# Optimization experiments

Hardware: AMD Instinct MI355X
Metric: run time of the kernel (lower is better)

## Reference

```python
import jax, jax.numpy as jnp
import numpy as np

PAD = float(-2**32 + 1)


def setup_inputs() -> dict:
    key = jax.random.key(0)
    ks = jax.random.split(key, 10)
    B, S, D = 8, 1024, 1024
    s = 0.02  # keep projections in sane range
    return {
        "Q": jax.random.normal(ks[0], (B, S, D), jnp.float32),
        "K": jax.random.normal(ks[1], (B, S, D), jnp.float32),
        "V": jax.random.normal(ks[2], (B, S, D), jnp.float32),
        "WQ": jax.random.normal(ks[3], (D, D), jnp.float32) * s,
        "bQ": jnp.zeros((D,), jnp.float32),
        "WK": jax.random.normal(ks[4], (D, D), jnp.float32) * s,
        "bK": jnp.zeros((D,), jnp.float32),
        "WV": jax.random.normal(ks[5], (D, D), jnp.float32) * s,
        "bV": jnp.zeros((D,), jnp.float32),
        "WO": jax.random.normal(ks[6], (D, D), jnp.float32) * s,
        "bO": jnp.zeros((D,), jnp.float32),
        "h": 16,
    }


def reference(Q, K, V, WQ, bQ, WK, bK, WV, bV, WO, bO, h):
    B, S, D = Q.shape
    dk = D // h
    # Dense projections with relu activation (as in the Keras layer)
    Qp = jax.nn.relu(Q @ WQ + bQ)
    Kp = jax.nn.relu(K @ WK + bK)
    Vp = jax.nn.relu(V @ WV + bV)
    # tf.concat(tf.split(x, h, axis=2), axis=0): head-major stacking -> (h, B, S, dk)
    qh = Qp.reshape(B, S, h, dk).transpose(2, 0, 1, 3)
    kh = Kp.reshape(B, S, h, dk).transpose(2, 0, 1, 3)
    vh = Vp.reshape(B, S, h, dk).transpose(2, 0, 1, 3)
    # scaled dot product; NOTE: source scales by 1/sqrt(d_model), not 1/sqrt(d_k)
    scores = jnp.einsum('hbqd,hbkd->hbqk', qh, kh) / jnp.sqrt(jnp.float32(D))
    # key padding mask: zero key rows -> large negative
    kmask = jnp.sum(jnp.abs(kh), axis=-1) != 0  # (h,B,Tk)
    scores = jnp.where(kmask[:, :, None, :], scores, PAD)
    w = jax.nn.softmax(scores, axis=-1)
    # query padding mask: zero query rows -> zero weights
    qmask = jnp.sign(jnp.sum(jnp.abs(qh), axis=-1))  # (h,B,Tq), 0/1
    w = w * qmask[:, :, :, None]
    # dropout_prob = 0.0 -> identity
    out = jnp.einsum('hbqk,hbkd->hbqd', w, vh)
    # tf.concat(tf.split(dot_product, h, axis=0), axis=2) -> (B,S,h*dk)
    out = out.transpose(1, 2, 0, 3).reshape(B, S, D)
    return jax.nn.relu(out @ WO + bO)
```

## Files before the change

kernel.cpp:

```cpp
#include <hip/hip_runtime.h>
#include <hip/hip_bf16.h>
#include <cstdint>

#define DEV __device__ __forceinline__

typedef __attribute__((ext_vector_type(4))) float f32x4;
typedef __attribute__((ext_vector_type(8))) short b16x8;
typedef __attribute__((ext_vector_type(4))) unsigned short u16x4;
typedef __attribute__((ext_vector_type(8))) unsigned short u16x8;
typedef __attribute__((ext_vector_type(2))) unsigned int u32x2;
typedef __attribute__((ext_vector_type(4))) unsigned int u32x4;

typedef __attribute__((address_space(1))) void gvoid_t;
typedef __attribute__((address_space(3))) void lvoid_t;

static constexpr int Bsz = 8, Ssz = 1024, Dsz = 1024;
static constexpr int Mrows = Bsz * Ssz;

DEV void gld16(const void* g, void* l) {
  __builtin_amdgcn_global_load_lds((gvoid_t*)(uintptr_t)g,
                                   (lvoid_t*)(unsigned)(uintptr_t)l, 16, 0, 0);
}

DEV unsigned short f2bf(float x) {
  unsigned int u = __float_as_uint(x);
  u += 0x7fffu + ((u >> 16) & 1u);
  return (unsigned short)(u >> 16);
}

DEV unsigned int cvt2(float lo, float hi) {
  __hip_bfloat162 h = __float22bfloat162_rn(make_float2(lo, hi));
  unsigned int u;
  __builtin_memcpy(&u, &h, 4);
  return u;
}

DEV float fexp2(float x) {
#if __has_builtin(__builtin_amdgcn_exp2f)
  return __builtin_amdgcn_exp2f(x);
#else
  return exp2f(x);
#endif
}

__global__ __launch_bounds__(256) void wconv_kernel(
    const float* __restrict__ WQ, const float* __restrict__ WK,
    const float* __restrict__ WV, const float* __restrict__ WO,
    unsigned short* __restrict__ Wt) {
  __shared__ float tile[64][65];
  const int w = blockIdx.z;
  const float* W = (w == 0) ? WQ : (w == 1) ? WK : (w == 2) ? WV : WO;
  const int k0 = blockIdx.x * 64, n0 = blockIdx.y * 64;
  const int t = threadIdx.x;
  {
    const int r = t >> 4;
    const int c = (t & 15) * 4;
#pragma unroll
    for (int i = 0; i < 4; ++i) {
      f32x4 v = *(const f32x4*)(W + (size_t)(k0 + i * 16 + r) * Dsz + n0 + c);
      tile[i * 16 + r][c + 0] = v[0];
      tile[i * 16 + r][c + 1] = v[1];
      tile[i * 16 + r][c + 2] = v[2];
      tile[i * 16 + r][c + 3] = v[3];
    }
  }
  __syncthreads();
  {
    const int n = t >> 2;
    const int ks = (t & 3) * 16;
    unsigned short* dst =
        Wt + (size_t)w * Dsz * Dsz + (size_t)(n0 + n) * Dsz + k0 + ks;
#pragma unroll
    for (int j = 0; j < 16; j += 4) {
      u16x4 p;
#pragma unroll
      for (int jj = 0; jj < 4; ++jj) p[jj] = f2bf(tile[ks + j + jj][n]);
      *(u16x4*)(dst + j) = p;
    }
  }
}

template <int OUT_MODE>
DEV void gemm_body_f32(unsigned short* __restrict__ Asl,
                       unsigned short* __restrict__ Bsl,
                       const float* __restrict__ A,
                       const unsigned short* __restrict__ Bt,
                       const float* __restrict__ bias, void* __restrict__ C_,
                       int m0, int n0, float outscale) {
  constexpr int Kd = 1024, Nd = 1024;
  const int t = threadIdx.x, lane = t & 63, wave = t >> 6;
  const int grp = lane >> 4, r16 = lane & 15;
  const int wm = wave >> 2, wn = wave & 3;
  const int swz = (r16 & 7) << 4;
  f32x4 acc[4][4] = {};
  f32x4 areg[2][2];

  auto loadA = [&](int kt) {
#pragma unroll
    for (int it = 0; it < 2; ++it) {
      int chunk = it * 512 + t;
      int row = chunk >> 3, c = chunk & 7;
      int csw = c ^ (row & 7);
      const float* src = A + (size_t)(m0 + row) * Kd + kt + csw * 8;
      areg[it][0] = *(const f32x4*)src;
      areg[it][1] = *(const f32x4*)(src + 4);
    }
  };
  auto writeA = [&]() {
#pragma unroll
    for (int it = 0; it < 2; ++it) {
      int chunk = it * 512 + t;
      u32x4 w;
      w[0] = cvt2(areg[it][0][0], areg[it][0][1]);
      w[1] = cvt2(areg[it][0][2], areg[it][0][3]);
      w[2] = cvt2(areg[it][1][0], areg[it][1][1]);
      w[3] = cvt2(areg[it][1][2], areg[it][1][3]);
      *(u32x4*)((char*)Asl + chunk * 16) = w;
    }
  };
  auto stageB = [&](int kt, int pb) {
#pragma unroll
    for (int j = 0; j < 4; ++j) {
      int chunk = (wave * 4 + j) * 64 + lane;
      int row = chunk >> 3, c = chunk & 7;
      int csw = c ^ (row & 7);
      gld16(Bt + (size_t)(n0 + row) * Kd + kt + csw * 8,
            (char*)Bsl + pb * 32768 + (wave * 4 + j) * 1024);
    }
  };

  loadA(0);
  stageB(0, 0);
  int cur = 0;
  for (int kt = 0; kt < Kd; kt += 64) {
    writeA();
    __syncthreads();
    if (kt < Kd - 64) {
      stageB(kt + 64, cur ^ 1);
      loadA(kt + 64);
    }
#pragma unroll
    for (int cs = 0; cs < 2; ++cs) {
      b16x8 af[4], bfr[4];
#pragma unroll
      for (int mi = 0; mi < 4; ++mi)
        af[mi] = *(const b16x8*)((char*)Asl + (wm * 64 + mi * 16 + r16) * 128 +
                                 ((cs * 64 + grp * 16) ^ swz));
#pragma unroll
      for (int ni = 0; ni < 4; ++ni)
        bfr[ni] = *(const b16x8*)((char*)Bsl + cur * 32768 +
                                  (wn * 64 + ni * 16 + r16) * 128 +
                                  ((cs * 64 + grp * 16) ^ swz));
#pragma unroll
      for (int mi = 0; mi < 4; ++mi)
#pragma unroll
        for (int ni = 0; ni < 4; ++ni)
          acc[mi][ni] = __builtin_amdgcn_mfma_f32_16x16x32_bf16(
              af[mi], bfr[ni], acc[mi][ni], 0, 0, 0);
    }
    __syncthreads();
    cur ^= 1;
  }
#pragma unroll
  for (int mi = 0; mi < 4; ++mi) {
#pragma unroll
    for (int ni = 0; ni < 4; ++ni) {
      int col = n0 + wn * 64 + ni * 16 + r16;
      float bv = bias[col];
      int row0 = m0 + wm * 64 + mi * 16 + grp * 4;
      if constexpr (OUT_MODE == 2) {
        int bb = row0 >> 10, s = row0 & 1023;
        u16x4 pk;
#pragma unroll
        for (int r = 0; r < 4; ++r)
          pk[r] = f2bf(fmaxf(acc[mi][ni][r] + bv, 0.0f) * outscale);
        *(u16x4*)((unsigned short*)C_ +
                  (((size_t)(bb * 1024 + col)) << 10) + s) = pk;
      } else {
#pragma unroll
        for (int r = 0; r < 4; ++r) {
          float v = fmaxf(acc[mi][ni][r] + bv, 0.0f) * outscale;
          ((unsigned short*)C_)[(size_t)(row0 + r) * Nd + col] = f2bf(v);
        }
      }
    }
  }
}

DEV void gemm_body_bf16(unsigned short* __restrict__ Asl,
                        unsigned short* __restrict__ Bsl,
                        const unsigned short* __restrict__ A,
                        const unsigned short* __restrict__ Bt,
                        const float* __restrict__ bias, float* __restrict__ C_,
                        int m0, int n0) {
  constexpr int Kd = 1024, Nd = 1024;
  const int t = threadIdx.x, lane = t & 63, wave = t >> 6;
  const int grp = lane >> 4, r16 = lane & 15;
  const int wm = wave >> 1, wn = wave & 1;
  const int swz = (r16 & 7) << 4;
  f32x4 acc[4][4] = {};
  for (int kt = 0; kt < Kd; kt += 64) {
#pragma unroll
    for (int j = 0; j < 4; ++j) {
      int chunk = (wave * 4 + j) * 64 + lane;
      int row = chunk >> 3, c = chunk & 7;
      int csw = c ^ (row & 7);
      gld16(Bt + (size_t)(n0 + row) * Kd + kt + csw * 8,
            (char*)Bsl + (wave * 4 + j) * 1024);
      gld16(A + (size_t)(m0 + row) * Kd + kt + csw * 8,
            (char*)Asl + (wave * 4 + j) * 1024);
    }
    __syncthreads();
#pragma unroll
    for (int cs = 0; cs < 2; ++cs) {
      b16x8 af[4], bfr[4];
#pragma unroll
      for (int mi = 0; mi < 4; ++mi)
        af[mi] = *(const b16x8*)((char*)Asl + (wm * 64 + mi * 16 + r16) * 128 +
                                 ((cs * 64 + grp * 16) ^ swz));
#pragma unroll
      for (int ni = 0; ni < 4; ++ni)
        bfr[ni] = *(const b16x8*)((char*)Bsl + (wn * 64 + ni * 16 + r16) * 128 +
                                  ((cs * 64 + grp * 16) ^ swz));
#pragma unroll
      for (int mi = 0; mi < 4; ++mi)
#pragma unroll
        for (int ni = 0; ni < 4; ++ni)
          acc[mi][ni] = __builtin_amdgcn_mfma_f32_16x16x32_bf16(
              af[mi], bfr[ni], acc[mi][ni], 0, 0, 0);
    }
    __syncthreads();
  }
#pragma unroll
  for (int mi = 0; mi < 4; ++mi) {
#pragma unroll
    for (int ni = 0; ni < 4; ++ni) {
      int col = n0 + wn * 64 + ni * 16 + r16;
      float bv = bias[col];
      int row0 = m0 + wm * 64 + mi * 16 + grp * 4;
#pragma unroll
      for (int r = 0; r < 4; ++r) {
        float v = fmaxf(acc[mi][ni][r] + bv, 0.0f);
        C_[(size_t)(row0 + r) * Nd + col] = v;
      }
    }
  }
}

static constexpr float QSCALE = 0.03125f * 1.4426950408889634f;

__global__ __launch_bounds__(512) void proj3_kernel(
    const float* __restrict__ Q, const float* __restrict__ K,
    const float* __restrict__ V, const unsigned short* __restrict__ Wt,
    const float* __restrict__ bQ, const float* __restrict__ bK,
    const float* __restrict__ bV, unsigned short* __restrict__ Qp,
    unsigned short* __restrict__ Kp, unsigned short* __restrict__ VpT) {
  __shared__ unsigned short Asl[128 * 64] __attribute__((aligned(16)));
  __shared__ unsigned short Bsl[2 * 256 * 64] __attribute__((aligned(16)));
  const size_t DD = (size_t)Dsz * Dsz;
  const int bid = blockIdx.x;
  const int id2 = (bid & 7) * 32 + (bid >> 3);
  const int n0 = (id2 & 3) * 256, m0 = (id2 >> 2) * 128;
  const int z = blockIdx.z;
  if (z == 0)
    gemm_body_f32<1>(Asl, Bsl, Q, Wt, bQ, Qp, m0, n0, QSCALE);
  else if (z == 1)
    gemm_body_f32<1>(Asl, Bsl, K, Wt + DD, bK, Kp, m0, n0, 1.0f);
  else
    gemm_body_f32<2>(Asl, Bsl, V, Wt + 2 * DD, bV, VpT, m0, n0, 1.0f);
}

__global__ __launch_bounds__(256) void out_gemm_kernel(
    const unsigned short* __restrict__ AO,
    const unsigned short* __restrict__ WOt, const float* __restrict__ bO,
    float* __restrict__ Out) {
  __shared__ unsigned short Asl[128 * 64] __attribute__((aligned(16)));
  __shared__ unsigned short Bsl[128 * 64] __attribute__((aligned(16)));
  const int bid = blockIdx.x;
  const int id2 = (bid & 7) * 64 + (bid >> 3);
  const int n0 = (id2 & 7) * 128, m0 = (id2 >> 3) * 128;
  gemm_body_bf16(Asl, Bsl, AO, WOt, bO, Out, m0, n0);
}

__global__ __launch_bounds__(512, 4) void attn_kernel(
    const unsigned short* __restrict__ Qp, const unsigned short* __restrict__ Kp,
    const unsigned short* __restrict__ VpT, unsigned short* __restrict__ AO) {
  __shared__ unsigned short Ks[2][64 * 64] __attribute__((aligned(16)));
  __shared__ unsigned short Vs[2][64 * 64] __attribute__((aligned(16)));
  __shared__ unsigned short Ps[16][16 * 64] __attribute__((aligned(16)));
  const int t = threadIdx.x, lane = t & 63, wave = t >> 6;
  const int grp = lane >> 4, r16 = lane & 15;
  const int bid = blockIdx.x;
  const int id2 = (bid & 7) * 64 + (bid >> 3);
  const int q0 = (id2 & 3) * 256;
  const int bh = id2 >> 2;
  const int b = bh & 7, head = bh >> 3;

  const int srow = t >> 3, scc = t & 7;
  const int csw = scc ^ (srow & 7);
  const unsigned short* kbase = Kp + ((size_t)b * Ssz) * Dsz + head * 64;
  const unsigned short* vbase = VpT + ((size_t)b * Dsz + head * 64) * Ssz;

  const int sqA = q0 + wave * 16 + r16;
  const unsigned short* qbA = Qp + ((size_t)b * Ssz + sqA) * Dsz + head * 64;
  const unsigned short* qbB = qbA + (size_t)128 * Dsz;
  b16x8 qfA0 = *(const b16x8*)(qbA + grp * 8);
  b16x8 qfA1 = *(const b16x8*)(qbA + 32 + grp * 8);
  b16x8 qfB0 = *(const b16x8*)(qbB + grp * 8);
  b16x8 qfB1 = *(const b16x8*)(qbB + 32 + grp * 8);

  f32x4 oA[4] = {}, oB[4] = {};
  f32x4 olA = {}, olB = {};
  const f32x4 zero4 = {0.0f, 0.0f, 0.0f, 0.0f};
  const b16x8 ones = {16256, 16256, 16256, 16256,
                      16256, 16256, 16256, 16256};

  auto stage = [&](int kv0, int pb) {
    gld16(kbase + (size_t)(kv0 + srow) * Dsz + csw * 8,
          (char*)Ks[pb] + wave * 1024);
    gld16(vbase + (size_t)srow * Ssz + kv0 + csw * 8,
          (char*)Vs[pb] + wave * 1024);
  };

  stage(0, 0);
  __syncthreads();
  int cur = 0;

  for (int it = 0; it < 16; ++it) {
    if (it < 15) stage((it + 1) * 64, cur ^ 1);

    __builtin_amdgcn_s_setprio(1);
    f32x4 scA[4], scB[4];
#pragma unroll
    for (int f = 0; f < 4; ++f) {
      int k = f * 16 + r16;
      int kswz = (k & 7) << 4;
      const char* kb = (const char*)Ks[cur] + k * 128;
      b16x8 kf0 = *(const b16x8*)(kb + ((grp * 16) ^ kswz));
      b16x8 kf1 = *(const b16x8*)(kb + ((64 + grp * 16) ^ kswz));
      f32x4 sA = __builtin_amdgcn_mfma_f32_16x16x32_bf16(kf0, qfA0, zero4, 0, 0, 0);
      scA[f] = __builtin_amdgcn_mfma_f32_16x16x32_bf16(kf1, qfA1, sA, 0, 0, 0);
      f32x4 sB = __builtin_amdgcn_mfma_f32_16x16x32_bf16(kf0, qfB0, zero4, 0, 0, 0);
      scB[f] = __builtin_amdgcn_mfma_f32_16x16x32_bf16(kf1, qfB1, sB, 0, 0, 0);
    }
    __builtin_amdgcn_s_setprio(0);

    {
      int qs = (r16 & 7) << 4;
      char* prowA = (char*)Ps + (wave * 2 + 0) * 2048 + r16 * 128;
      char* prowB = (char*)Ps + (wave * 2 + 1) * 2048 + r16 * 128;
#pragma unroll
      for (int f = 0; f < 4; ++f) {
        u32x2 w;
        w[0] = cvt2(fexp2(scA[f][0]), fexp2(scA[f][1]));
        w[1] = cvt2(fexp2(scA[f][2]), fexp2(scA[f][3]));
        *(u32x2*)(prowA + ((f * 32 + grp * 8) ^ qs)) = w;
      }
#pragma unroll
      for (int f = 0; f < 4; ++f) {
        u32x2 w;
        w[0] = cvt2(fexp2(scB[f][0]), fexp2(scB[f][1]));
        w[1] = cvt2(fexp2(scB[f][2]), fexp2(scB[f][3]));
        *(u32x2*)(prowB + ((f * 32 + grp * 8) ^ qs)) = w;
      }
    }

    __builtin_amdgcn_s_setprio(1);
#pragma unroll
    for (int ks = 0; ks < 2; ++ks) {
      int pswz = (r16 & 7) << 4;
      int poff = r16 * 128 + ((ks * 64 + grp * 16) ^ pswz);
      b16x8 paA = *(const b16x8*)((char*)Ps + (wave * 2 + 0) * 2048 + poff);
      b16x8 paB = *(const b16x8*)((char*)Ps + (wave * 2 + 1) * 2048 + poff);
      olA = __builtin_amdgcn_mfma_f32_16x16x32_bf16(paA, ones, olA, 0, 0, 0);
      olB = __builtin_amdgcn_mfma_f32_16x16x32_bf16(paB, ones, olB, 0, 0, 0);
#pragma unroll
      for (int fc = 0; fc < 4; ++fc) {
        int d = fc * 16 + r16;
        int vswz = (d & 7) << 4;
        b16x8 vb = *(const b16x8*)((char*)Vs[cur] + d * 128 +
                                   ((ks * 64 + grp * 16) ^ vswz));
        oA[fc] = __builtin_amdgcn_mfma_f32_16x16x32_bf16(paA, vb, oA[fc], 0, 0, 0);
        oB[fc] = __builtin_amdgcn_mfma_f32_16x16x32_bf16(paB, vb, oB[fc], 0, 0, 0);
      }
    }
    __builtin_amdgcn_s_setprio(0);
    __syncthreads();
    cur ^= 1;
  }

#pragma unroll
  for (int fc = 0; fc < 4; ++fc) {
    int col = head * 64 + fc * 16 + r16;
#pragma unroll
    for (int r = 0; r < 4; ++r) {
      int rowA = q0 + wave * 16 + grp * 4 + r;
      AO[((size_t)b * Ssz + rowA) * Dsz + col] = f2bf(oA[fc][r] / olA[r]);
      AO[((size_t)b * Ssz + rowA + 128) * Dsz + col] = f2bf(oB[fc][r] / olB[r]);
    }
  }
}

extern "C" void kernel_launch(void* const* d_in, const int* in_sizes, int n_in,
                              void* d_out, int out_size, void* d_ws,
                              size_t ws_size, hipStream_t stream) {
  const float* Q = (const float*)d_in[0];
  const float* K = (const float*)d_in[1];
  const float* V = (const float*)d_in[2];
  const float* WQ = (const float*)d_in[3];
  const float* bQ = (const float*)d_in[4];
  const float* WK = (const float*)d_in[5];
  const float* bK = (const float*)d_in[6];
  const float* WV = (const float*)d_in[7];
  const float* bV = (const float*)d_in[8];
  const float* WO = (const float*)d_in[9];
  const float* bO = (const float*)d_in[10];

  char* ws = (char*)d_ws;
  const size_t MB = 1024ull * 1024ull;
  const size_t DD = (size_t)Dsz * Dsz;
  unsigned short* Wt = (unsigned short*)(ws);
  unsigned short* Qp = (unsigned short*)(ws + 8 * MB);
  unsigned short* Kp = (unsigned short*)(ws + 24 * MB);
  unsigned short* VpT = (unsigned short*)(ws + 40 * MB);
  unsigned short* AO = (unsigned short*)(ws + 56 * MB);

  wconv_kernel<<<dim3(16, 16, 4), 256, 0, stream>>>(WQ, WK, WV, WO, Wt);
  proj3_kernel<<<dim3(256, 1, 3), 512, 0, stream>>>(Q, K, V, Wt, bQ, bK, bV,
                                                    Qp, Kp, VpT);
  attn_kernel<<<512, 512, 0, stream>>>(Qp, Kp, VpT, AO);
  out_gemm_kernel<<<512, 256, 0, stream>>>(AO, Wt + 3 * DD, bO, (float*)d_out);
}
```

Before: 154.7 us.

## Prefetch A tiles two stages ahead with manual waitcnt and raw barriers

The projection GEMM's fp32 A-operand register prefetch gains a second register bank, so global loads for tile k+2 are issued while tile k is being computed. `__syncthreads` is replaced by explicit `s_waitcnt vmcnt`/`lgkmcnt` plus `s_barrier`, with `sched_barrier` fences to pin the issue order. The goal is to hide global load latency of the fp32 A stream behind the MFMA work. In exchange it uses more VGPRs, which may lower occupancy, and it relies on hand-counted vmcnt values matching the load issue order.

```diff
diff --git a/kernel.cpp b/kernel.cpp
--- a/kernel.cpp
+++ b/kernel.cpp
@@ -42,6 +42,16 @@
   return exp2f(x);
 #endif
 }
+
+#define WAIT_LGKM0                                     \
+  asm volatile("s_waitcnt lgkmcnt(0)" ::: "memory");   \
+  __builtin_amdgcn_sched_barrier(0)
+#define WAIT_VM(N)                                         \
+  asm volatile("s_waitcnt vmcnt(" #N ")" ::: "memory");    \
+  __builtin_amdgcn_sched_barrier(0)
+#define RAW_BAR                       \
+  __builtin_amdgcn_s_barrier();       \
+  __builtin_amdgcn_sched_barrier(0)
 
 __global__ __launch_bounds__(256) void wconv_kernel(
     const float* __restrict__ WQ, const float* __restrict__ WK,
@@ -93,28 +103,28 @@
   const int wm = wave >> 2, wn = wave & 3;
   const int swz = (r16 & 7) << 4;
   f32x4 acc[4][4] = {};
-  f32x4 areg[2][2];
-
-  auto loadA = [&](int kt) {
+  f32x4 areg[2][2][2];
+
+  auto loadA = [&](int kt, int bank) {
 #pragma unroll
     for (int it = 0; it < 2; ++it) {
       int chunk = it * 512 + t;
       int row = chunk >> 3, c = chunk & 7;
       int csw = c ^ (row & 7);
       const float* src = A + (size_t)(m0 + row) * Kd + kt + csw * 8;
-      areg[it][0] = *(const f32x4*)src;
-      areg[it][1] = *(const f32x4*)(src + 4);
+      areg[bank][it][0] = *(const f32x4*)src;
+      areg[bank][it][1] = *(const f32x4*)(src + 4);
     }
   };
-  auto writeA = [&]() {
+  auto writeA = [&](int bank) {
 #pragma unroll
     for (int it = 0; it < 2; ++it) {
       int chunk = it * 512 + t;
       u32x4 w;
-      w[0] = cvt2(areg[it][0][0], areg[it][0][1]);
-      w[1] = cvt2(areg[it][0][2], areg[it][0][3]);
-      w[2] = cvt2(areg[it][1][0], areg[it][1][1]);
-      w[3] = cvt2(areg[it][1][2], areg[it][1][3]);
+      w[0] = cvt2(areg[bank][it][0][0], areg[bank][it][0][1]);
+      w[1] = cvt2(areg[bank][it][0][2], areg[bank][it][0][3]);
+      w[2] = cvt2(areg[bank][it][1][0], areg[bank][it][1][1]);
+      w[3] = cvt2(areg[bank][it][1][2], areg[bank][it][1][3]);
       *(u32x4*)((char*)Asl + chunk * 16) = w;
     }
   };
@@ -129,15 +139,29 @@
     }
   };
 
-  loadA(0);
+  loadA(0, 0);
+  __builtin_amdgcn_sched_barrier(0);
   stageB(0, 0);
+  __builtin_amdgcn_sched_barrier(0);
+  loadA(64, 1);
+  __builtin_amdgcn_sched_barrier(0);
+
   int cur = 0;
   for (int kt = 0; kt < Kd; kt += 64) {
-    writeA();
-    __syncthreads();
+    const int bank = (kt >> 6) & 1;
+    writeA(bank);
+    if (kt == Kd - 64) {
+      WAIT_VM(0);
+    } else {
+      WAIT_VM(4);
+    }
+    WAIT_LGKM0;
+    RAW_BAR;
     if (kt < Kd - 64) {
       stageB(kt + 64, cur ^ 1);
-      loadA(kt + 64);
+      __builtin_amdgcn_sched_barrier(0);
+      if (kt < Kd - 128) loadA(kt + 128, bank);
+      __builtin_amdgcn_sched_barrier(0);
     }
 #pragma unroll
     for (int cs = 0; cs < 2; ++cs) {
@@ -158,7 +182,8 @@
           acc[mi][ni] = __builtin_amdgcn_mfma_f32_16x16x32_bf16(
               af[mi], bfr[ni], acc[mi][ni], 0, 0, 0);
     }
-    __syncthreads();
+    WAIT_LGKM0;
+    RAW_BAR;
     cur ^= 1;
   }
 #pragma unroll
```

Result: slower. 182.1 us (+17.7%).
